# Kernel tuning notes

Measured on AMD Instinct MI355X. Metric: run time of the kernel, lower is better.

Reference implementation:

```python
import jax, jax.numpy as jnp
import numpy as np

B, T, H, E = 8, 2048, 512, 512

def setup_inputs() -> dict:
    key = jax.random.key(0)
    k1, k2, k3, k4 = jax.random.split(key, 4)
    tokens = jax.random.normal(k1, (B, T, H), dtype=jnp.float32)
    # Linear(hidden,embed,bias=False): stored as (in,out) so Q = tokens @ Wq
    Wq = jax.random.normal(k2, (H, E), dtype=jnp.float32) / np.sqrt(H)
    Wk = jax.random.normal(k3, (H, E), dtype=jnp.float32) / np.sqrt(H)
    Wv = jax.random.normal(k4, (H, H), dtype=jnp.float32) / np.sqrt(H)
    return {"tokens": tokens, "Wq": Wq, "Wk": Wk, "Wv": Wv}

def reference(tokens, Wq, Wk, Wv):
    Q = jnp.einsum('bth,he->bte', tokens, Wq)   # [B,T,E]
    K = jnp.einsum('bsh,he->bse', tokens, Wk)   # [B,T,E]
    V = jnp.einsum('bsh,hd->bsd', tokens, Wv)   # [B,T,H]
    scoremats = jnp.einsum('bte,bse->bts', Q, K)  # [B,T,T]
    # NOTE: softmax over axis=1 (query axis t), matching F.softmax(dim=1)
    attnmats = jax.nn.softmax(scoremats, axis=1)
    ctx_vecs = jnp.einsum('bts,bsh->bth', attnmats, V)  # [B,T,H]
    return ctx_vecs
```

## Files before the change

kernel.cpp:

```cpp
#include <hip/hip_runtime.h>

typedef _Float16 f16;
typedef _Float16 f16x8 __attribute__((ext_vector_type(8)));
typedef _Float16 f16x4 __attribute__((ext_vector_type(4)));
typedef float   f32x4 __attribute__((ext_vector_type(4)));

#define LOG2E 1.44269504088896340736f

__device__ __forceinline__ f32x4 mfma_f16(f16x8 a, f16x8 b, f32x4 c){
  return __builtin_amdgcn_mfma_f32_16x16x32_f16(a, b, c, 0, 0, 0);
}
__device__ __forceinline__ float fexp2(float x){ return __builtin_amdgcn_exp2f(x); }

__device__ __forceinline__ void gld16(void* lds, const void* g){
  __builtin_amdgcn_global_load_lds(
      (const __attribute__((address_space(1))) unsigned int*)g,
      (__attribute__((address_space(3))) unsigned int*)lds,
      16, 0, 0);
}


__global__ __launch_bounds__(256) void k_prep_g(const float* __restrict__ Wq,
                                                const float* __restrict__ Wk,
                                                f16* __restrict__ B16){
  __shared__ float ak[32][36];
  __shared__ float aq[32][36];
  const int n0 = blockIdx.y * 32, e0 = blockIdx.x * 32;
  const int u = threadIdx.x;
  const int ty = u >> 4, tx = u & 15;
  float acc[2][2] = {};
  for (int x0 = 0; x0 < 512; x0 += 32){
    __syncthreads();
    {
      int r = u >> 3, c4 = (u & 7) * 4;
      *(float4*)&ak[r][c4] = *(const float4*)&Wk[(n0 + r) * 512 + x0 + c4];
      *(float4*)&aq[r][c4] = *(const float4*)&Wq[(e0 + r) * 512 + x0 + c4];
    }
    __syncthreads();
#pragma unroll 8
    for (int x = 0; x < 32; ++x){
      float k0 = ak[ty * 2 + 0][x], k1 = ak[ty * 2 + 1][x];
      float q0 = aq[tx * 2 + 0][x], q1 = aq[tx * 2 + 1][x];
      acc[0][0] += k0 * q0; acc[0][1] += k0 * q1;
      acc[1][0] += k1 * q0; acc[1][1] += k1 * q1;
    }
  }
#pragma unroll
  for (int i = 0; i < 2; ++i)
#pragma unroll
    for (int j = 0; j < 2; ++j)
      B16[(size_t)(n0 + ty * 2 + i) * 512 + e0 + tx * 2 + j] = (f16)acc[i][j];
}

__global__ __launch_bounds__(256) void k_prep_wv(const float* __restrict__ Wv,
                                                 f16* __restrict__ B16){
  __shared__ float t[64][72];
  const int e0 = blockIdx.x * 64, h0 = blockIdx.y * 64;
  const int u = threadIdx.x;
#pragma unroll
  for (int k = 0; k < 4; ++k){
    int idx = u + k * 256; int r = idx >> 4, c4 = (idx & 15) * 4;
    *(float4*)&t[r][c4] = *(const float4*)&Wv[(e0 + r) * 512 + h0 + c4];
  }
  __syncthreads();
#pragma unroll
  for (int k = 0; k < 4; ++k){
    int idx = u + k * 256; int j = idx >> 4, i4 = (idx & 15) * 4;
#pragma unroll
    for (int c = 0; c < 4; ++c)
      B16[(size_t)(512 + h0 + j) * 512 + e0 + i4 + c] = (f16)t[i4 + c][j];
  }
}

__global__ __launch_bounds__(256) void k_cast(const float* __restrict__ tok,
                                              f16* __restrict__ T16){
  int i = blockIdx.x * 256 + threadIdx.x;
  const float4* p = (const float4*)tok + (size_t)i * 2;
  float4 a = p[0], b = p[1];
  f16x8 h;
  h[0] = (f16)a.x; h[1] = (f16)a.y; h[2] = (f16)a.z; h[3] = (f16)a.w;
  h[4] = (f16)b.x; h[5] = (f16)b.y; h[6] = (f16)b.z; h[7] = (f16)b.w;
  *((f16x8*)T16 + i) = h;
}

__global__ __launch_bounds__(256, 4) void k_gemm(const f16* __restrict__ T16,
                                                 const f16* __restrict__ B16,
                                                 f16* __restrict__ QG,
                                                 f16* __restrict__ VT){
  __shared__ __align__(16) f16 Abuf[128 * 64];
  __shared__ __align__(16) f16 Bbuf[128 * 64];
  const int tb = blockIdx.x, nb = blockIdx.y;
  const int u = threadIdx.x;
  const int w = u >> 6, l = u & 63, lr = l & 15, lq = l >> 4;
  const int sx8 = (l & 7) ^ (l >> 3), hi8 = l >> 3;
  const int wm = (w & 1) * 64, wn = (w >> 1) * 64;
  f32x4 acc[4][4] = {};
  const f16* sa0 = T16 + (size_t)tb * 128 * 512;
  const f16* sb0 = B16 + (size_t)nb * 128 * 512;
  for (int c = 0; c < 8; ++c){
    {
      const f16* sa = sa0 + c * 64;
      const f16* sb_ = sb0 + c * 64;
#pragma unroll
      for (int k = 0; k < 4; ++k){
        int i = w * 4 + k;
        int row = i * 8 + hi8;
        gld16((char*)Abuf + i * 1024, sa  + (size_t)row * 512 + sx8 * 8);
        gld16((char*)Bbuf + i * 1024, sb_ + (size_t)row * 512 + sx8 * 8);
      }
    }
    __syncthreads();
#pragma unroll
    for (int es = 0; es < 2; ++es){
      f16x8 af[4], bf[4];
#pragma unroll
      for (int mt = 0; mt < 4; ++mt){
        int row = wm + mt * 16 + lr;
        af[mt] = *(const f16x8*)((const char*)Abuf + row * 128 + (((es * 4 + lq) ^ (row & 7)) << 4));
      }
#pragma unroll
      for (int nt = 0; nt < 4; ++nt){
        int row = wn + nt * 16 + lr;
        bf[nt] = *(const f16x8*)((const char*)Bbuf + row * 128 + (((es * 4 + lq) ^ (row & 7)) << 4));
      }
#pragma unroll
      for (int mt = 0; mt < 4; ++mt)
#pragma unroll
        for (int nt = 0; nt < 4; ++nt)
          acc[mt][nt] = mfma_f16(af[mt], bf[nt], acc[mt][nt]);
    }
    __syncthreads();
  }
  if (nb < 4){
#pragma unroll
    for (int mt = 0; mt < 4; ++mt)
#pragma unroll
      for (int nt = 0; nt < 4; ++nt){
        int n = nb * 128 + wn + nt * 16 + lr;
        int r0 = tb * 128 + wm + mt * 16 + lq * 4;
#pragma unroll
        for (int j = 0; j < 4; ++j)
          QG[(size_t)(r0 + j) * 512 + n] = (f16)acc[mt][nt][j];
      }
  } else {
#pragma unroll
    for (int mt = 0; mt < 4; ++mt)
#pragma unroll
      for (int nt = 0; nt < 4; ++nt){
        int h = (nb - 4) * 128 + wn + nt * 16 + lr;
        int r0 = tb * 128 + wm + mt * 16 + lq * 4;
        int bq = r0 >> 11, s = r0 & 2047;
        f16x4 hv;
#pragma unroll
        for (int j = 0; j < 4; ++j) hv[j] = (f16)acc[mt][nt][j];
        *(f16x4*)&VT[(size_t)(bq * 512 + h) * 2048 + s] = hv;
      }
  }
}

__global__ __launch_bounds__(512, 2) void k_pass1p(const f16* __restrict__ T16,
                                                   const f16* __restrict__ QG,
                                                   f16* __restrict__ Pp,
                                                   float* __restrict__ Mp,
                                                   float* __restrict__ Dp){
  const int gid = blockIdx.x;
  const int b = gid & 7;
  const int sb = (gid >> 3) & 15;
  const int tb = gid >> 7;
  const int u = threadIdx.x;
  const int w = u >> 6, l = u & 63, lr = l & 15, lq = l >> 4;
  const int sx8 = (l & 7) ^ (l >> 3), hi8 = l >> 3;
  const int ws2 = w & 1, wt2 = w >> 1;
  const int wm = ws2 * 64, wn = wt2 * 64;

  __shared__ __align__(16) f16 Abuf[128 * 64];
  __shared__ __align__(16) f16 Bbuf[256 * 64];
  __shared__ float redM[4][128];
  __shared__ float redD[4][128];

  f32x4 acc[4][4] = {};
  const f16* sa0 = T16 + ((size_t)(b * 2048 + sb * 128) * 512);
  const f16* sb0 = QG + ((size_t)(b * 2048 + tb * 256) * 512);
  for (int c = 0; c < 8; ++c){
    {
      const f16* sa = sa0 + c * 64;
      const f16* sb_ = sb0 + c * 64;
#pragma unroll
      for (int k = 0; k < 2; ++k){
        int i = w * 2 + k;
        int row = i * 8 + hi8;
        gld16((char*)Abuf + i * 1024, sa + (size_t)row * 512 + sx8 * 8);
      }
#pragma unroll
      for (int k = 0; k < 4; ++k){
        int i = w * 4 + k;
        int row = i * 8 + hi8;
        gld16((char*)Bbuf + i * 1024, sb_ + (size_t)row * 512 + sx8 * 8);
      }
    }
    __syncthreads();
#pragma unroll
    for (int es = 0; es < 2; ++es){
      f16x8 af[4], bf[4];
#pragma unroll
      for (int mt = 0; mt < 4; ++mt){
        int row = wm + mt * 16 + lr;
        af[mt] = *(const f16x8*)((const char*)Abuf + row * 128 + (((es * 4 + lq) ^ (row & 7)) << 4));
      }
#pragma unroll
      for (int nt = 0; nt < 4; ++nt){
        int row = wn + nt * 16 + lr;
        bf[nt] = *(const f16x8*)((const char*)Bbuf + row * 128 + (((es * 4 + lq) ^ (row & 7)) << 4));
      }
#pragma unroll
      for (int mt = 0; mt < 4; ++mt)
#pragma unroll
        for (int nt = 0; nt < 4; ++nt)
          acc[mt][nt] = mfma_f16(af[mt], bf[nt], acc[mt][nt]);
    }
    __syncthreads();
  }
#pragma unroll
  for (int mt = 0; mt < 4; ++mt)
#pragma unroll
    for (int nt = 0; nt < 4; ++nt)
#pragma unroll
      for (int j = 0; j < 4; ++j)
        acc[mt][nt][j] *= LOG2E;
#pragma unroll
  for (int mt = 0; mt < 4; ++mt)
#pragma unroll
    for (int j = 0; j < 4; ++j){
      float m2 = fmaxf(fmaxf(acc[mt][0][j], acc[mt][1][j]),
                       fmaxf(acc[mt][2][j], acc[mt][3][j]));
#pragma unroll
      for (int off = 1; off <= 8; off <<= 1)
        m2 = fmaxf(m2, __shfl_xor(m2, off, 64));
      if (lr == 0) redM[wt2][wm + mt * 16 + lq * 4 + j] = m2;
    }
  __syncthreads();
  float M[4][4];
#pragma unroll
  for (int mt = 0; mt < 4; ++mt)
#pragma unroll
    for (int j = 0; j < 4; ++j){
      int idx = wm + mt * 16 + lq * 4 + j;
      M[mt][j] = fmaxf(fmaxf(redM[0][idx], redM[1][idx]),
                       fmaxf(redM[2][idx], redM[3][idx]));
    }
#pragma unroll
  for (int mt = 0; mt < 4; ++mt)
#pragma unroll
    for (int nt = 0; nt < 4; ++nt){
      int t = tb * 256 + wn + nt * 16 + lr;
      f16x4 h4;
#pragma unroll
      for (int j = 0; j < 4; ++j){
        float p = fexp2(acc[mt][nt][j] - M[mt][j]);
        acc[mt][nt][j] = p;
        h4[j] = (f16)p;
      }
      *(f16x4*)&Pp[(size_t)(b * 2048 + t) * 2048 + sb * 128 + wm + mt * 16 + lq * 4] = h4;
    }
#pragma unroll
  for (int mt = 0; mt < 4; ++mt)
#pragma unroll
    for (int j = 0; j < 4; ++j){
      float sd = acc[mt][0][j] + acc[mt][1][j] + acc[mt][2][j] + acc[mt][3][j];
#pragma unroll
      for (int off = 1; off <= 8; off <<= 1)
        sd += __shfl_xor(sd, off, 64);
      if (lr == 0) redD[wt2][wm + mt * 16 + lq * 4 + j] = sd;
    }
  __syncthreads();
  if (u < 128){
    int sg = b * 2048 + sb * 128 + u;
    Mp[tb * 16384 + sg] = fmaxf(fmaxf(redM[0][u], redM[1][u]),
                                fmaxf(redM[2][u], redM[3][u]));
    Dp[tb * 16384 + sg] = redD[0][u] + redD[1][u] + redD[2][u] + redD[3][u];
  }
}

__global__ __launch_bounds__(256) void k_scm(const float* __restrict__ Mp,
                                             const float* __restrict__ Dp,
                                             f16* __restrict__ SC16){
  int i = blockIdx.x * 256 + threadIdx.x;
  float mv[8];
  float m = -1e30f;
#pragma unroll
  for (int ti = 0; ti < 8; ++ti){
    mv[ti] = Mp[ti * 16384 + i];
    m = fmaxf(m, mv[ti]);
  }
  float d = 0.f;
#pragma unroll
  for (int ti = 0; ti < 8; ++ti)
    d += Dp[ti * 16384 + i] * fexp2(mv[ti] - m);
  float rd = 1.0f / d;
#pragma unroll
  for (int ti = 0; ti < 8; ++ti)
    SC16[ti * 16384 + i] = (f16)(fexp2(mv[ti] - m) * rd);
}

__global__ __launch_bounds__(256, 4) void k_pass2p(const f16* __restrict__ Pp,
                                                   const f16* __restrict__ VT,
                                                   const f16* __restrict__ SC16,
                                                   float* __restrict__ out){
  const int gid = blockIdx.x;
  const int b = gid & 7;
  const int tb = (gid >> 3) & 15;
  const int hb = gid >> 7;
  const int ti = tb >> 1;
  const int u = threadIdx.x;
  const int w = u >> 6, l = u & 63, lr = l & 15, lq = l >> 4;
  const int sx8 = (l & 7) ^ (l >> 3), hi8 = l >> 3;

  __shared__ __align__(16) f16 Abuf[64 * 64];
  __shared__ __align__(16) f16 Bbuf[128 * 64];
  __shared__ __align__(16) f16 scl[2048];

  {
    f16x8 v = *(const f16x8*)&SC16[(size_t)ti * 16384 + b * 2048 + u * 8];
    *(f16x8*)&scl[u * 8] = v;
  }
  f32x4 acc[4][2] = {};
  const f16* sa0 = VT + ((size_t)(b * 512 + hb * 64) * 2048);
  const f16* sb0 = Pp + ((size_t)(b * 2048 + tb * 128) * 2048);
  for (int c = 0; c < 32; ++c){
    {
      const f16* sa = sa0 + c * 64;
      const f16* sb_ = sb0 + c * 64;
#pragma unroll
      for (int k = 0; k < 2; ++k){
        int i = w * 2 + k;
        int row = i * 8 + hi8;
        gld16((char*)Abuf + i * 1024, sa + (size_t)row * 2048 + sx8 * 8);
      }
#pragma unroll
      for (int k = 0; k < 4; ++k){
        int i = w * 4 + k;
        int row = i * 8 + hi8;
        gld16((char*)Bbuf + i * 1024, sb_ + (size_t)row * 2048 + sx8 * 8);
      }
    }
    __syncthreads();
#pragma unroll
    for (int es = 0; es < 2; ++es){
      f16x8 sclv = *(const f16x8*)&scl[c * 64 + es * 32 + lq * 8];
      f16x8 af[4], bf[2];
#pragma unroll
      for (int ht = 0; ht < 4; ++ht){
        int row = ht * 16 + lr;
        af[ht] = *(const f16x8*)((const char*)Abuf + row * 128 + (((es * 4 + lq) ^ (row & 7)) << 4));
      }
#pragma unroll
      for (int nt = 0; nt < 2; ++nt){
        int row = w * 32 + nt * 16 + lr;
        f16x8 p = *(const f16x8*)((const char*)Bbuf + row * 128 + (((es * 4 + lq) ^ (row & 7)) << 4));
        bf[nt] = p * sclv;
      }
#pragma unroll
      for (int ht = 0; ht < 4; ++ht)
#pragma unroll
        for (int nt = 0; nt < 2; ++nt)
          acc[ht][nt] = mfma_f16(af[ht], bf[nt], acc[ht][nt]);
    }
    __syncthreads();
  }
#pragma unroll
  for (int ht = 0; ht < 4; ++ht)
#pragma unroll
    for (int nt = 0; nt < 2; ++nt){
      int t = tb * 128 + w * 32 + nt * 16 + lr;
      int h = hb * 64 + ht * 16 + lq * 4;
      float4 v;
      v.x = acc[ht][nt][0]; v.y = acc[ht][nt][1];
      v.z = acc[ht][nt][2]; v.w = acc[ht][nt][3];
      *(float4*)&out[(size_t)(b * 2048 + t) * 512 + h] = v;
    }
}

extern "C" void kernel_launch(void* const* d_in, const int* in_sizes, int n_in,
                              void* d_out, int out_size, void* d_ws, size_t ws_size,
                              hipStream_t stream){
  (void)in_sizes; (void)n_in; (void)out_size; (void)ws_size;
  const float* tokens = (const float*)d_in[0];
  const float* Wq = (const float*)d_in[1];
  const float* Wk = (const float*)d_in[2];
  const float* Wv = (const float*)d_in[3];
  char* ws = (char*)d_ws;
  f16*    T16 = (f16*)(ws);
  f16*    QG  = (f16*)(ws + (16u << 20));
  f16*    VT  = (f16*)(ws + (32u << 20));
  f16*    B16 = (f16*)(ws + (48u << 20));
  f16*    SC16= (f16*)(ws + (50u << 20));
  float*  Mp  = (float*)(ws + (51u << 20));
  float*  Dp  = (float*)(ws + (52u << 20));
  f16*    Pp  = (f16*)(ws + (54u << 20));
  float* out = (float*)d_out;

  k_prep_g <<<dim3(16, 16), dim3(256), 0, stream>>>(Wq, Wk, B16);
  k_prep_wv<<<dim3(8, 8),   dim3(256), 0, stream>>>(Wv, B16);
  k_cast   <<<dim3(4096),   dim3(256), 0, stream>>>(tokens, T16);
  k_gemm   <<<dim3(128, 8), dim3(256), 0, stream>>>(T16, B16, QG, VT);
  k_pass1p <<<dim3(1024),   dim3(512), 0, stream>>>(T16, QG, Pp, Mp, Dp);
  k_scm    <<<dim3(64),     dim3(256), 0, stream>>>(Mp, Dp, SC16);
  k_pass2p <<<dim3(1024),   dim3(256), 0, stream>>>(Pp, VT, SC16, out);
}
```

Measured before the change: 162.1 us.

## Double-buffer pass1 LDS tiles with half-width K chunks to overlap loads

Splits the K dimension of the pass-1 score GEMM into 16 chunks of 32 instead of 8 of 64. The A and B LDS tiles are now double-buffered, so the global-to-LDS load of the next chunk is issued before the MFMAs on the current chunk. This halves the barriers per chunk and aims to hide global load latency behind compute. In exchange there are twice as many iterations, each with a smaller MFMA body, and a new XOR swizzle for the 64-byte rows, which changes the LDS bank pattern.

```diff
diff --git a/kernel.cpp b/kernel.cpp
--- a/kernel.cpp
+++ b/kernel.cpp
@@ -169,56 +169,54 @@
   const int tb = gid >> 7;
   const int u = threadIdx.x;
   const int w = u >> 6, l = u & 63, lr = l & 15, lq = l >> 4;
-  const int sx8 = (l & 7) ^ (l >> 3), hi8 = l >> 3;
+  const int sx4 = (l & 3) ^ ((l >> 3) & 3), hi4 = l >> 2;
   const int ws2 = w & 1, wt2 = w >> 1;
   const int wm = ws2 * 64, wn = wt2 * 64;
 
-  __shared__ __align__(16) f16 Abuf[128 * 64];
-  __shared__ __align__(16) f16 Bbuf[256 * 64];
+  __shared__ __align__(16) f16 Abuf[2][128 * 32];
+  __shared__ __align__(16) f16 Bbuf[2][256 * 32];
   __shared__ float redM[4][128];
   __shared__ float redD[4][128];
 
   f32x4 acc[4][4] = {};
   const f16* sa0 = T16 + ((size_t)(b * 2048 + sb * 128) * 512);
   const f16* sb0 = QG + ((size_t)(b * 2048 + tb * 256) * 512);
-  for (int c = 0; c < 8; ++c){
+  auto stage = [&](int c, int buf){
+    const f16* sa = sa0 + c * 32;
+    const f16* sb_ = sb0 + c * 32;
     {
-      const f16* sa = sa0 + c * 64;
-      const f16* sb_ = sb0 + c * 64;
-#pragma unroll
-      for (int k = 0; k < 2; ++k){
-        int i = w * 2 + k;
-        int row = i * 8 + hi8;
-        gld16((char*)Abuf + i * 1024, sa + (size_t)row * 512 + sx8 * 8);
-      }
-#pragma unroll
-      for (int k = 0; k < 4; ++k){
-        int i = w * 4 + k;
-        int row = i * 8 + hi8;
-        gld16((char*)Bbuf + i * 1024, sb_ + (size_t)row * 512 + sx8 * 8);
-      }
-    }
-    __syncthreads();
-#pragma unroll
-    for (int es = 0; es < 2; ++es){
-      f16x8 af[4], bf[4];
-#pragma unroll
-      for (int mt = 0; mt < 4; ++mt){
-        int row = wm + mt * 16 + lr;
-        af[mt] = *(const f16x8*)((const char*)Abuf + row * 128 + (((es * 4 + lq) ^ (row & 7)) << 4));
-      }
-#pragma unroll
-      for (int nt = 0; nt < 4; ++nt){
-        int row = wn + nt * 16 + lr;
-        bf[nt] = *(const f16x8*)((const char*)Bbuf + row * 128 + (((es * 4 + lq) ^ (row & 7)) << 4));
-      }
-#pragma unroll
-      for (int mt = 0; mt < 4; ++mt)
-#pragma unroll
-        for (int nt = 0; nt < 4; ++nt)
-          acc[mt][nt] = mfma_f16(af[mt], bf[nt], acc[mt][nt]);
-    }
-    __syncthreads();
+      int row = w * 16 + hi4;
+      gld16((char*)&Abuf[buf][0] + w * 1024, sa + (size_t)row * 512 + sx4 * 8);
+    }
+#pragma unroll
+    for (int k = 0; k < 2; ++k){
+      int i = w * 2 + k;
+      int row = i * 16 + hi4;
+      gld16((char*)&Bbuf[buf][0] + i * 1024, sb_ + (size_t)row * 512 + sx4 * 8);
+    }
+  };
+  stage(0, 0);
+  for (int c = 0; c < 16; ++c){
+    __syncthreads();
+    if (c < 15) stage(c + 1, (c + 1) & 1);
+    const f16* A = &Abuf[c & 1][0];
+    const f16* B = &Bbuf[c & 1][0];
+    f16x8 af[4], bf[4];
+#pragma unroll
+    for (int mt = 0; mt < 4; ++mt){
+      int row = wm + mt * 16 + lr;
+      af[mt] = *(const f16x8*)((const char*)A + row * 64 + ((lq ^ ((row >> 1) & 3)) << 4));
+    }
+#pragma unroll
+    for (int nt = 0; nt < 4; ++nt){
+      int row = wn + nt * 16 + lr;
+      bf[nt] = *(const f16x8*)((const char*)B + row * 64 + ((lq ^ ((row >> 1) & 3)) << 4));
+    }
+#pragma unroll
+    for (int mt = 0; mt < 4; ++mt)
+#pragma unroll
+      for (int nt = 0; nt < 4; ++nt)
+        acc[mt][nt] = mfma_f16(af[mt], bf[nt], acc[mt][nt]);
   }
 #pragma unroll
   for (int mt = 0; mt < 4; ++mt)
```

Result: slower. 198.8 us (+22.7%).
